# Kernel optimization log

Measured on AMD Instinct MI355X. Metric: run time of the kernel, lower is better.

## Reference

```python
import jax, jax.numpy as jnp
import numpy as np

N_NODES = 50000
N_EDGES = 800000
DIM = 128
N_LAYERS = 5
BN_EPS = 1e-3  # keras BatchNormalization default epsilon


def setup_inputs() -> dict:
    key = jax.random.key(0)
    ks = jax.random.split(key, 6)
    scale = 1.0 / np.sqrt(DIM)
    return {
        "x": jax.random.normal(ks[0], (N_NODES, DIM), dtype=jnp.float32),
        "edge_src": jax.random.randint(ks[1], (N_EDGES,), 0, N_NODES, dtype=jnp.int32),
        "edge_dst": jax.random.randint(ks[2], (N_EDGES,), 0, N_NODES, dtype=jnp.int32),
        "eps": jnp.zeros((N_LAYERS,), dtype=jnp.float32),
        "W1": jax.random.normal(ks[3], (N_LAYERS, DIM, DIM), dtype=jnp.float32) * scale,
        "b1": jnp.zeros((N_LAYERS, DIM), dtype=jnp.float32),
        "W2": jax.random.normal(ks[4], (N_LAYERS, DIM, DIM), dtype=jnp.float32) * scale,
        "b2": jnp.zeros((N_LAYERS, DIM), dtype=jnp.float32),
        "gamma": jnp.ones((N_LAYERS, DIM), dtype=jnp.float32),
        "beta": jnp.zeros((N_LAYERS, DIM), dtype=jnp.float32),
        "bn_mean": jnp.zeros((N_LAYERS, DIM), dtype=jnp.float32),
        "bn_var": jnp.ones((N_LAYERS, DIM), dtype=jnp.float32),
    }


def reference(x, edge_src, edge_dst, eps, W1, b1, W2, b2, gamma, beta, bn_mean, bn_var):
    n = x.shape[0]
    num_layers = W1.shape[0]
    hidden_rep = [x]
    h = x
    for l in range(num_layers):
        # sparse Adj @ h as gather + segment-sum (sum neighbor pooling)
        msgs = jnp.take(h, edge_src, axis=0)                       # [E, D]
        pooled = jax.ops.segment_sum(msgs, edge_dst, num_segments=n)  # [N, D]
        pooled = pooled + (1.0 + eps[l]) * h                        # GIN eps term
        # 2-layer MLP: Linear -> ReLU -> Linear
        z = jax.nn.relu(pooled @ W1[l] + b1[l])
        z = z @ W2[l] + b2[l]
        # BatchNorm (inference: moving statistics)
        z = gamma[l] * (z - bn_mean[l]) * jax.lax.rsqrt(bn_var[l] + BN_EPS) + beta[l]
        h = jax.nn.relu(z)
        hidden_rep.append(h)
    return tuple(hidden_rep)
```

## Files before the change

kernel.cpp:

```cpp
#include <hip/hip_runtime.h>
#include <hip/hip_bf16.h>

#define N_NODES 50000
#define N_EDGES 800000
#define DIM 128
#define N_LAYERS 5
#define BN_EPS 1e-3f

typedef __attribute__((ext_vector_type(8))) short bf16x8;
typedef __attribute__((ext_vector_type(4))) float f32x4;

__device__ __forceinline__ unsigned short f2bf(float f) {
    unsigned int v = __builtin_bit_cast(unsigned int, f);
    v += 0x7fffu + ((v >> 16) & 1u);
    return (unsigned short)(v >> 16);
}
__device__ __forceinline__ float bflo(unsigned int v) {
    return __builtin_bit_cast(float, v << 16);
}
__device__ __forceinline__ float bfhi(unsigned int v) {
    return __builtin_bit_cast(float, v & 0xffff0000u);
}


__global__ void init_zero_kernel(const float* __restrict__ x, float* __restrict__ out,
                                 unsigned short* __restrict__ hb, int* __restrict__ cnt) {
    int t = blockIdx.x * blockDim.x + threadIdx.x;
    if (t < (N_NODES * DIM) / 4) {
        f32x4 v = ((const f32x4*)x)[t];
        __builtin_nontemporal_store(v, (f32x4*)out + t);
        unsigned short u[4] = {f2bf(v.x), f2bf(v.y), f2bf(v.z), f2bf(v.w)};
        *(uint2*)(hb + t * 4) = *(uint2*)u;
    }
    int z = t - (N_NODES * DIM) / 4;
    if (z >= 0 && z < N_NODES) cnt[z] = 0;
}

__global__ void hist_kernel(const int* __restrict__ dst, int* __restrict__ cnt) {
    int e = blockIdx.x * blockDim.x + threadIdx.x;
    if (e < N_EDGES) atomicAdd(&cnt[dst[e]], 1);
}

__global__ __launch_bounds__(1024) void scan_kernel(const int* __restrict__ cnt,
                                                    int* __restrict__ row_start,
                                                    int* __restrict__ cursor) {
    __shared__ int wsum[16];
    __shared__ int s_carry;
    const int tid = threadIdx.x;
    const int lane = tid & 63, wave = tid >> 6;
    if (tid == 0) s_carry = 0;
    __syncthreads();
    for (int base = 0; base < N_NODES; base += 4096) {
        int i0 = base + tid * 4;
        int v[4];
#pragma unroll
        for (int j = 0; j < 4; j++) {
            int i = i0 + j;
            v[j] = (i < N_NODES) ? cnt[i] : 0;
        }
        int s = v[0] + v[1] + v[2] + v[3];
        int x = s;
#pragma unroll
        for (int off = 1; off < 64; off <<= 1) {
            int t = __shfl_up(x, off, 64);
            if (lane >= off) x += t;
        }
        if (lane == 63) wsum[wave] = x;
        __syncthreads();
        if (wave == 0) {
            int w = (lane < 16) ? wsum[lane] : 0;
#pragma unroll
            for (int off = 1; off < 16; off <<= 1) {
                int t = __shfl_up(w, off, 64);
                if (lane >= off) w += t;
            }
            if (lane < 16) wsum[lane] = w;
        }
        __syncthreads();
        int waveoff = (wave > 0) ? wsum[wave - 1] : 0;
        int carry = s_carry;
        int run = carry + waveoff + (x - s);
#pragma unroll
        for (int j = 0; j < 4; j++) {
            int i = i0 + j;
            if (i < N_NODES) { row_start[i] = run; cursor[i] = run; }
            run += v[j];
        }
        __syncthreads();
        if (tid == 1023) s_carry = carry + wsum[15];
        __syncthreads();
    }
    if (tid == 0) row_start[N_NODES] = s_carry;
}

__global__ void fill_kernel(const int* __restrict__ src, const int* __restrict__ dst,
                            int* __restrict__ cursor, int* __restrict__ col) {
    int e = blockIdx.x * blockDim.x + threadIdx.x;
    if (e < N_EDGES) {
        int d = dst[e];
        int pos = atomicAdd(&cursor[d], 1);
        col[pos] = src[e];
    }
}

__global__ void prep_kernel(const float* __restrict__ W1, const float* __restrict__ W2,
                            unsigned short* __restrict__ wp,
                            const float* __restrict__ gamma, const float* __restrict__ beta,
                            const float* __restrict__ mean, const float* __restrict__ var,
                            float* __restrict__ scale, float* __restrict__ shift) {
    int t = blockIdx.x * blockDim.x + threadIdx.x;
    if (t < N_LAYERS * 2 * 2048) {
        int mat = t >> 11;
        int r = t & 2047;
        int ks = r >> 9, nt = (r >> 6) & 7, lane = r & 63;
        int layer = mat >> 1;
        const float* W = ((mat & 1) ? W2 : W1) + layer * DIM * DIM;
        int n = nt * 16 + (lane & 15);
        int kb = ks * 32 + (lane >> 4) * 8;
        unsigned short u[8];
#pragma unroll
        for (int j = 0; j < 8; j++) u[j] = f2bf(W[(kb + j) * DIM + n]);
        *(uint4*)(wp + (size_t)mat * 16384 + ((ks * 8 + nt) * 64 + lane) * 8) = *(uint4*)u;
    }
    int i = t - N_LAYERS * 2 * 2048;
    if (i >= 0 && i < N_LAYERS * DIM) {
        float sc = gamma[i] * rsqrtf(var[i] + BN_EPS);
        scale[i] = sc;
        shift[i] = beta[i] - mean[i] * sc;
    }
}


__device__ __forceinline__ void acc8(float* a, uint4 v, float m) {
    a[0] = fmaf(m, bflo(v.x), a[0]); a[1] = fmaf(m, bfhi(v.x), a[1]);
    a[2] = fmaf(m, bflo(v.y), a[2]); a[3] = fmaf(m, bfhi(v.y), a[3]);
    a[4] = fmaf(m, bflo(v.z), a[4]); a[5] = fmaf(m, bfhi(v.z), a[5]);
    a[6] = fmaf(m, bflo(v.w), a[6]); a[7] = fmaf(m, bfhi(v.w), a[7]);
}

__global__ __launch_bounds__(256) void pool_kernel(const unsigned short* __restrict__ hb,
                                                   const int* __restrict__ row_start,
                                                   const int* __restrict__ col,
                                                   const float* __restrict__ eps_l,
                                                   unsigned short* __restrict__ pooled_b) {
    const int wave = threadIdx.x >> 6, lane = threadIdx.x & 63;
    const int n = blockIdx.x * 4 + wave;
    if (n >= N_NODES) return;
    const int nu = __builtin_amdgcn_readfirstlane(n);
    const float ev = 1.0f + eps_l[0];
    const int s0 = row_start[nu], s1 = row_start[nu + 1];
    const int q = lane >> 4;
    const int t = lane & 15;

    uint4 sv = *(const uint4*)(hb + (size_t)nu * DIM + t * 8);
    float a[8] = {0.f, 0.f, 0.f, 0.f, 0.f, 0.f, 0.f, 0.f};
    acc8(a, sv, (q == 0) ? ev : 0.f);

    for (int base = s0; base < s1; base += 64) {
        const int rem = s1 - base;
        const int nn = rem < 64 ? rem : 64;
        int ci = (base + lane < s1) ? __builtin_nontemporal_load(&col[base + lane]) : 0;
        for (int j = 0; j < nn; j += 24) {
            uint4 v[6];
#pragma unroll
            for (int i = 0; i < 6; i++) {
                if (j + i * 4 < nn) {
                    int idx = j + i * 4 + q;
                    idx = idx < 63 ? idx : 63;
                    int r = __shfl(ci, idx, 64);
                    v[i] = *(const uint4*)(hb + (size_t)r * DIM + t * 8);
                }
            }
#pragma unroll
            for (int i = 0; i < 6; i++) {
                if (j + i * 4 < nn) {
                    float m = (j + i * 4 + q < nn) ? 1.f : 0.f;
                    acc8(a, v[i], m);
                }
            }
        }
    }

#pragma unroll
    for (int k = 0; k < 8; k++) {
        a[k] += __shfl_xor(a[k], 16, 64);
        a[k] += __shfl_xor(a[k], 32, 64);
    }
    if (q == 0) {
        unsigned short u[8];
#pragma unroll
        for (int k = 0; k < 8; k++) u[k] = f2bf(a[k]);
        *(uint4*)(pooled_b + (size_t)nu * DIM + t * 8) = *(uint4*)u;
    }
}

__global__ __launch_bounds__(256) void mlp_kernel(
    const unsigned short* __restrict__ pooled_b,
    const unsigned short* __restrict__ wp1,
    const unsigned short* __restrict__ wp2,
    const float* __restrict__ b1,
    const float* __restrict__ b2,
    const float* __restrict__ bnscale,
    const float* __restrict__ bnshift,
    float* __restrict__ h_out,
    unsigned short* __restrict__ hb_out) {
    __shared__ __align__(16) unsigned short zfrag[4][4][64][8];
    const int tid = threadIdx.x;
    const int wave = tid >> 6, lane = tid & 63;
    const int m0 = blockIdx.x * 64;
    const int colc = lane & 15;
    const int quad = lane >> 4;
    const int arow = m0 + wave * 16 + colc;
    const int arow_c = arow < N_NODES ? arow : N_NODES - 1;

    bf16x8 a[4];
#pragma unroll
    for (int ks = 0; ks < 4; ks++)
        a[ks] = *(const bf16x8*)(pooled_b + arow_c * DIM + ks * 32 + quad * 8);

    f32x4 acc[8];
#pragma unroll
    for (int nt = 0; nt < 8; nt++) {
        acc[nt] = (f32x4){0.f, 0.f, 0.f, 0.f};
#pragma unroll
        for (int ks = 0; ks < 4; ks++) {
            bf16x8 b = *(const bf16x8*)(wp1 + ((ks * 8 + nt) * 64 + lane) * 8);
            acc[nt] = __builtin_amdgcn_mfma_f32_16x16x32_bf16(a[ks], b, acc[nt], 0, 0, 0);
        }
    }

#pragma unroll
    for (int nt = 0; nt < 8; nt++) {
        int n = nt * 16 + colc;
        float bias = b1[n];
#pragma unroll
        for (int r = 0; r < 4; r++) {
            float v = acc[nt][r] + bias;
            v = v > 0.f ? v : 0.f;
            int row16 = quad * 4 + r;
            zfrag[wave][n >> 5][(((n >> 3) & 3) << 4) | row16][n & 7] = f2bf(v);
        }
    }

#pragma unroll
    for (int ks = 0; ks < 4; ks++) a[ks] = *(const bf16x8*)(&zfrag[wave][ks][lane][0]);

    f32x4 acc2[8];
#pragma unroll
    for (int nt = 0; nt < 8; nt++) {
        acc2[nt] = (f32x4){0.f, 0.f, 0.f, 0.f};
#pragma unroll
        for (int ks = 0; ks < 4; ks++) {
            bf16x8 b = *(const bf16x8*)(wp2 + ((ks * 8 + nt) * 64 + lane) * 8);
            acc2[nt] = __builtin_amdgcn_mfma_f32_16x16x32_bf16(a[ks], b, acc2[nt], 0, 0, 0);
        }
    }

#pragma unroll
    for (int nt = 0; nt < 8; nt++) {
        int n = nt * 16 + colc;
        float bias = b2[n];
        float sc = bnscale[n], sh = bnshift[n];
#pragma unroll
        for (int r = 0; r < 4; r++) {
            int row = m0 + wave * 16 + quad * 4 + r;
            if (row < N_NODES) {
                float z = acc2[nt][r] + bias;
                z = z * sc + sh;
                z = z > 0.f ? z : 0.f;
                __builtin_nontemporal_store(z, &h_out[row * DIM + n]);
                hb_out[row * DIM + n] = f2bf(z);
            }
        }
    }
}


extern "C" void kernel_launch(void* const* d_in, const int* in_sizes, int n_in,
                              void* d_out, int out_size, void* d_ws, size_t ws_size,
                              hipStream_t stream) {
    const float* x     = (const float*)d_in[0];
    const int* esrc    = (const int*)d_in[1];
    const int* edst    = (const int*)d_in[2];
    const float* eps   = (const float*)d_in[3];
    const float* W1    = (const float*)d_in[4];
    const float* b1    = (const float*)d_in[5];
    const float* W2    = (const float*)d_in[6];
    const float* b2    = (const float*)d_in[7];
    const float* gam   = (const float*)d_in[8];
    const float* bet   = (const float*)d_in[9];
    const float* bmean = (const float*)d_in[10];
    const float* bvar  = (const float*)d_in[11];
    float* out = (float*)d_out;

    char* ws = (char*)d_ws;
    unsigned short* hb0   = (unsigned short*)(ws);
    unsigned short* hb1   = (unsigned short*)(ws + 12800000);
    int*   col        = (int*)  (ws + 25600000);
    int*   row_start  = (int*)  (ws + 28800000);
    int*   cursor     = (int*)  (ws + 29000192);
    int*   cnt        = (int*)  (ws + 29200384);
    unsigned short* wpack = (unsigned short*)(ws + 29400576);
    float* bnscale    = (float*)(ws + 29728256);
    float* bnshift    = (float*)(ws + 29730816);
    unsigned short* pooled_b = (unsigned short*)(ws + 29733376);

    init_zero_kernel<<<((N_NODES * DIM) / 4 + N_NODES + 255) / 256, 256, 0, stream>>>(
        x, out, hb0, cnt);
    hist_kernel<<<(N_EDGES + 255) / 256, 256, 0, stream>>>(edst, cnt);
    scan_kernel<<<1, 1024, 0, stream>>>(cnt, row_start, cursor);
    fill_kernel<<<(N_EDGES + 255) / 256, 256, 0, stream>>>(esrc, edst, cursor, col);
    prep_kernel<<<(N_LAYERS * 2 * 2048 + N_LAYERS * DIM + 255) / 256, 256, 0, stream>>>(
        W1, W2, wpack, gam, bet, bmean, bvar, bnscale, bnshift);

    const int pool_blocks = (N_NODES + 3) / 4;
    const int mlp_blocks  = (N_NODES + 63) / 64;
    unsigned short* hbuf[2] = {hb0, hb1};
    for (int l = 0; l < N_LAYERS; l++) {
        float* h_next = out + (size_t)(l + 1) * N_NODES * DIM;
        pool_kernel<<<pool_blocks, 256, 0, stream>>>(hbuf[l & 1], row_start, col, eps + l,
                                                     pooled_b);
        mlp_kernel<<<mlp_blocks, 256, 0, stream>>>(
            pooled_b,
            wpack + (size_t)(l * 2) * 16384,
            wpack + (size_t)(l * 2 + 1) * 16384,
            b1 + l * DIM, b2 + l * DIM,
            bnscale + l * DIM, bnshift + l * DIM,
            h_next, hbuf[(l + 1) & 1]);
    }
}
```

Before: 588.1 us.

## Split bf16 feature table into 32-column slices so each pool pass gathers from a smaller table

Stores the bf16 node features and pooled output as four column slices of 32 columns each, rather than one row-major 128-column table. Pool blocks now each handle one slice, so a gather pass touches a 3.2 MB table that fits in cache better, and each wave gathers 16 neighbors at a time with 64-byte rows. The cost is four times as many pool blocks, each re-reading the CSR indices, plus a wider cross-lane reduction. The MLP kernel's scattered 2-byte bf16 writes now go to strided slice addresses.

```diff
diff --git a/kernel.cpp b/kernel.cpp
--- a/kernel.cpp
+++ b/kernel.cpp
@@ -6,9 +6,14 @@
 #define DIM 128
 #define N_LAYERS 5
 #define BN_EPS 1e-3f
+#define NSLICE 4
+#define SLICE_COLS 32
+#define POOL_BLK_PER_SLICE 12500
 
 typedef __attribute__((ext_vector_type(8))) short bf16x8;
 typedef __attribute__((ext_vector_type(4))) float f32x4;
+typedef __attribute__((ext_vector_type(4))) unsigned int u32x4;
+typedef __attribute__((ext_vector_type(2))) unsigned int u32x2;
 
 __device__ __forceinline__ unsigned short f2bf(float f) {
     unsigned int v = __builtin_bit_cast(unsigned int, f);
@@ -30,7 +35,12 @@
         f32x4 v = ((const f32x4*)x)[t];
         __builtin_nontemporal_store(v, (f32x4*)out + t);
         unsigned short u[4] = {f2bf(v.x), f2bf(v.y), f2bf(v.z), f2bf(v.w)};
-        *(uint2*)(hb + t * 4) = *(uint2*)u;
+        int node = t >> 5;
+        int c = (t & 31) * 4;
+        int sl = c >> 5;
+        int w = c & 31;
+        *(u32x2*)(hb + (size_t)sl * N_NODES * SLICE_COLS + (size_t)node * SLICE_COLS + w) =
+            *(u32x2*)u;
     }
     int z = t - (N_NODES * DIM) / 4;
     if (z >= 0 && z < N_NODES) cnt[z] = 0;
@@ -120,7 +130,7 @@
         unsigned short u[8];
 #pragma unroll
         for (int j = 0; j < 8; j++) u[j] = f2bf(W[(kb + j) * DIM + n]);
-        *(uint4*)(wp + (size_t)mat * 16384 + ((ks * 8 + nt) * 64 + lane) * 8) = *(uint4*)u;
+        *(u32x4*)(wp + (size_t)mat * 16384 + ((ks * 8 + nt) * 64 + lane) * 8) = *(u32x4*)u;
     }
     int i = t - N_LAYERS * 2 * 2048;
     if (i >= 0 && i < N_LAYERS * DIM) {
@@ -131,71 +141,74 @@
 }
 
 
-__device__ __forceinline__ void acc8(float* a, uint4 v, float m) {
+__device__ __forceinline__ void acc8(float* a, u32x4 v, float m) {
     a[0] = fmaf(m, bflo(v.x), a[0]); a[1] = fmaf(m, bfhi(v.x), a[1]);
     a[2] = fmaf(m, bflo(v.y), a[2]); a[3] = fmaf(m, bfhi(v.y), a[3]);
     a[4] = fmaf(m, bflo(v.z), a[4]); a[5] = fmaf(m, bfhi(v.z), a[5]);
     a[6] = fmaf(m, bflo(v.w), a[6]); a[7] = fmaf(m, bfhi(v.w), a[7]);
 }
 
-__global__ __launch_bounds__(256) void pool_kernel(const unsigned short* __restrict__ hb,
+__global__ __launch_bounds__(256) void pool_kernel(const unsigned short* __restrict__ hbs,
                                                    const int* __restrict__ row_start,
                                                    const int* __restrict__ col,
                                                    const float* __restrict__ eps_l,
-                                                   unsigned short* __restrict__ pooled_b) {
+                                                   unsigned short* __restrict__ pooled_s) {
     const int wave = threadIdx.x >> 6, lane = threadIdx.x & 63;
-    const int n = blockIdx.x * 4 + wave;
-    if (n >= N_NODES) return;
-    const int nu = __builtin_amdgcn_readfirstlane(n);
+    const int bid = blockIdx.x;
+    const int slice = bid / POOL_BLK_PER_SLICE;
+    const int nb = bid - slice * POOL_BLK_PER_SLICE;
+    const int n = nb * 4 + wave;
+    const unsigned short* tab = hbs + (size_t)slice * N_NODES * SLICE_COLS;
     const float ev = 1.0f + eps_l[0];
-    const int s0 = row_start[nu], s1 = row_start[nu + 1];
-    const int q = lane >> 4;
-    const int t = lane & 15;
-
-    uint4 sv = *(const uint4*)(hb + (size_t)nu * DIM + t * 8);
+    const int s0 = row_start[n], s1 = row_start[n + 1];
+    const int g = lane >> 2;
+    const int t = lane & 3;
+
+    u32x4 sv = *(const u32x4*)(tab + (size_t)n * SLICE_COLS + t * 8);
     float a[8] = {0.f, 0.f, 0.f, 0.f, 0.f, 0.f, 0.f, 0.f};
-    acc8(a, sv, (q == 0) ? ev : 0.f);
+    acc8(a, sv, (g == 0) ? ev : 0.f);
 
     for (int base = s0; base < s1; base += 64) {
         const int rem = s1 - base;
         const int nn = rem < 64 ? rem : 64;
         int ci = (base + lane < s1) ? __builtin_nontemporal_load(&col[base + lane]) : 0;
-        for (int j = 0; j < nn; j += 24) {
-            uint4 v[6];
-#pragma unroll
-            for (int i = 0; i < 6; i++) {
-                if (j + i * 4 < nn) {
-                    int idx = j + i * 4 + q;
-                    idx = idx < 63 ? idx : 63;
-                    int r = __shfl(ci, idx, 64);
-                    v[i] = *(const uint4*)(hb + (size_t)r * DIM + t * 8);
-                }
+        u32x4 v[4];
+#pragma unroll
+        for (int i = 0; i < 4; i++) {
+            if (i * 16 < nn) {
+                int r = __shfl(ci, i * 16 + g, 64);
+                v[i] = *(const u32x4*)(tab + (size_t)r * SLICE_COLS + t * 8);
             }
-#pragma unroll
-            for (int i = 0; i < 6; i++) {
-                if (j + i * 4 < nn) {
-                    float m = (j + i * 4 + q < nn) ? 1.f : 0.f;
-                    acc8(a, v[i], m);
-                }
+        }
+#pragma unroll
+        for (int i = 0; i < 4; i++) {
+            if (i * 16 < nn) {
+                float m = (i * 16 + g < nn) ? 1.f : 0.f;
+                acc8(a, v[i], m);
             }
         }
     }
 
 #pragma unroll
     for (int k = 0; k < 8; k++) {
+        a[k] += __shfl_xor(a[k], 4, 64);
+        a[k] += __shfl_xor(a[k], 8, 64);
         a[k] += __shfl_xor(a[k], 16, 64);
         a[k] += __shfl_xor(a[k], 32, 64);
     }
-    if (q == 0) {
+    if (g == 0) {
         unsigned short u[8];
 #pragma unroll
         for (int k = 0; k < 8; k++) u[k] = f2bf(a[k]);
-        *(uint4*)(pooled_b + (size_t)nu * DIM + t * 8) = *(uint4*)u;
+        __builtin_nontemporal_store(
+            *(u32x4*)u,
+            (u32x4*)(pooled_s + (size_t)slice * N_NODES * SLICE_COLS +
+                     (size_t)n * SLICE_COLS + t * 8));
     }
 }
 
 __global__ __launch_bounds__(256) void mlp_kernel(
-    const unsigned short* __restrict__ pooled_b,
+    const unsigned short* __restrict__ pooled_s,
     const unsigned short* __restrict__ wp1,
     const unsigned short* __restrict__ wp2,
     const float* __restrict__ b1,
@@ -216,7 +229,8 @@
     bf16x8 a[4];
 #pragma unroll
     for (int ks = 0; ks < 4; ks++)
-        a[ks] = *(const bf16x8*)(pooled_b + arow_c * DIM + ks * 32 + quad * 8);
+        a[ks] = *(const bf16x8*)(pooled_s + (size_t)ks * N_NODES * SLICE_COLS +
+                                 (size_t)arow_c * SLICE_COLS + quad * 8);
 
     f32x4 acc[8];
 #pragma unroll
@@ -261,6 +275,8 @@
         int n = nt * 16 + colc;
         float bias = b2[n];
         float sc = bnscale[n], sh = bnshift[n];
+        unsigned short* hslice = hb_out + (size_t)(n >> 5) * N_NODES * SLICE_COLS;
+        int w = n & 31;
 #pragma unroll
         for (int r = 0; r < 4; r++) {
             int row = m0 + wave * 16 + quad * 4 + r;
@@ -269,7 +285,7 @@
                 z = z * sc + sh;
                 z = z > 0.f ? z : 0.f;
                 __builtin_nontemporal_store(z, &h_out[row * DIM + n]);
-                hb_out[row * DIM + n] = f2bf(z);
+                hslice[(size_t)row * SLICE_COLS + w] = f2bf(z);
             }
         }
     }
@@ -303,7 +319,7 @@
     unsigned short* wpack = (unsigned short*)(ws + 29400576);
     float* bnscale    = (float*)(ws + 29728256);
     float* bnshift    = (float*)(ws + 29730816);
-    unsigned short* pooled_b = (unsigned short*)(ws + 29733376);
+    unsigned short* pooled_s = (unsigned short*)(ws + 29733376);
 
     init_zero_kernel<<<((N_NODES * DIM) / 4 + N_NODES + 255) / 256, 256, 0, stream>>>(
         x, out, hb0, cnt);
@@ -313,15 +329,15 @@
     prep_kernel<<<(N_LAYERS * 2 * 2048 + N_LAYERS * DIM + 255) / 256, 256, 0, stream>>>(
         W1, W2, wpack, gam, bet, bmean, bvar, bnscale, bnshift);
 
-    const int pool_blocks = (N_NODES + 3) / 4;
+    const int pool_blocks = NSLICE * POOL_BLK_PER_SLICE;
     const int mlp_blocks  = (N_NODES + 63) / 64;
     unsigned short* hbuf[2] = {hb0, hb1};
     for (int l = 0; l < N_LAYERS; l++) {
         float* h_next = out + (size_t)(l + 1) * N_NODES * DIM;
         pool_kernel<<<pool_blocks, 256, 0, stream>>>(hbuf[l & 1], row_start, col, eps + l,
-                                                     pooled_b);
+                                                     pooled_s);
         mlp_kernel<<<mlp_blocks, 256, 0, stream>>>(
-            pooled_b,
+            pooled_s,
             wpack + (size_t)(l * 2) * 16384,
             wpack + (size_t)(l * 2 + 1) * 16384,
             b1 + l * DIM, b2 + l * DIM,
```

Result: slower. 820.8 us (+39.6%).
